# Performance work log

Measured on AMD Instinct MI355X. Metric: run time of the kernel, lower is better.

Reference implementation:

```python
import jax, jax.numpy as jnp
import numpy as np

DEGREE = 10

def _chebyshev_basis(x, degree):
    # x: [B, F] -> basis: [B, F, degree+1] via T0=1, T1=t, Tk=2t*T_{k-1}-T_{k-2}
    t = jnp.tanh(x)
    polys = [jnp.ones_like(t), t]
    for _ in range(2, degree + 1):
        polys.append(2.0 * t * polys[-1] - polys[-2])
    return jnp.stack(polys, axis=-1)

def setup_inputs() -> dict:
    key = jax.random.key(0)
    k1, k2, k3, k4 = jax.random.split(key, 4)
    B, F_IN, F_OUT, D = 8192, 1024, 1024, DEGREE
    x = jax.random.normal(k1, (B, F_IN), dtype=jnp.float32)
    coeff_mean = jax.random.normal(k2, (F_IN, F_OUT, D + 1), dtype=jnp.float32) * 0.05
    coeff_log_var = jnp.full((F_IN, F_OUT, D + 1), -5.0, dtype=jnp.float32)
    base_weight = jax.random.normal(k3, (F_IN, F_OUT), dtype=jnp.float32) * 0.05
    # reparameterization noise, n_samples=1
    eps = jax.random.normal(k4, (1, F_IN, F_OUT, D + 1), dtype=jnp.float32)
    return {"x": x, "coeff_mean": coeff_mean, "coeff_log_var": coeff_log_var,
            "base_weight": base_weight, "eps": eps}

def reference(x, coeff_mean, coeff_log_var, base_weight, eps):
    basis = _chebyshev_basis(x, DEGREE)                      # [B, F_in, D+1]
    std = jnp.exp(0.5 * coeff_log_var)                       # [F_in, F_out, D+1]
    coeffs = coeff_mean[None] + eps * std[None]              # [S, F_in, F_out, D+1]
    poly_out = jnp.einsum('bin,sion->bo', basis, coeffs) / coeffs.shape[0]
    linear_out = x @ base_weight
    # KL with prior_mean=0, prior_var=1 (prior_scale=1.0)
    var = jnp.exp(coeff_log_var)
    kl = 0.5 * jnp.sum(var + coeff_mean ** 2 - 1.0 - coeff_log_var)
    return poly_out + linear_out, kl
```

## Files before the change

### kernel.cpp

```cpp
#include <hip/hip_runtime.h>

#define MDIM 8192
#define NDIM 1024
#define FIN  1024
#define DP1  11
#define KDIM 11264
#define KHALF 5632
#define ROWB 22528
#define HOFS 2883584u
#define FGOFS 1441792u
#define NT 88
#define NITER 44

typedef __attribute__((ext_vector_type(8))) short short8;
typedef __attribute__((ext_vector_type(4))) float float4v;
typedef const __attribute__((address_space(1))) unsigned int* gptr_t;
typedef __attribute__((address_space(3))) unsigned int* lptr_t;

__device__ __forceinline__ unsigned int pk2(float a, float b) {
  unsigned int ua = __float_as_uint(a), ub = __float_as_uint(b);
  ua += 0x7FFFu + ((ua >> 16) & 1u);
  ub += 0x7FFFu + ((ub >> 16) & 1u);
  return __builtin_amdgcn_perm(ub, ua, 0x07060302);
}

__device__ __forceinline__ float fast_tanh(float x) {
  float e = __expf(2.f * x);
  return 1.f - 2.f / (e + 1.f);
}

struct Cheb { float t, T2, T3, T4, T5, T6, T7, T8, T9, T10; };
__device__ __forceinline__ Cheb cheb_eval(float x) {
  Cheb c;
  c.t = fast_tanh(x);
  const float t2 = 2.f * c.t;
  c.T2 = t2 * c.t - 1.f;
  c.T3 = t2 * c.T2 - c.t;
  c.T4 = t2 * c.T3 - c.T2;
  c.T5 = t2 * c.T4 - c.T3;
  c.T6 = t2 * c.T5 - c.T4;
  c.T7 = t2 * c.T6 - c.T5;
  c.T8 = t2 * c.T7 - c.T6;
  c.T9 = t2 * c.T8 - c.T7;
  c.T10 = t2 * c.T9 - c.T8;
  return c;
}

__device__ __forceinline__ void pack_pair(float xa, float xb, unsigned int* w) {
  Cheb a = cheb_eval(xa), b = cheb_eval(xb);
  w[0] = pk2(a.t, a.T2);  w[1] = pk2(a.T3, a.T4); w[2] = pk2(a.T5, a.T6);
  w[3] = pk2(a.T7, a.T8); w[4] = pk2(a.T9, a.T10); w[5] = pk2(xa, b.t);
  w[6] = pk2(b.T2, b.T3); w[7] = pk2(b.T4, b.T5);  w[8] = pk2(b.T6, b.T7);
  w[9] = pk2(b.T8, b.T9); w[10] = pk2(b.T10, xb);
}

__global__ __launch_bounds__(256) void prep_A_kernel(const float* __restrict__ x,
                                                     unsigned int* __restrict__ A) {
  __shared__ unsigned int rowbuf[5632];
  const int row = blockIdx.x;
  const int tid = threadIdx.x;
  float4 xv = ((const float4*)(x + (size_t)row * FIN))[tid];
  unsigned int w[22];
  pack_pair(xv.x, xv.y, w);
  pack_pair(xv.z, xv.w, w + 11);
#pragma unroll
  for (int j = 0; j < 22; j++) rowbuf[tid * 22 + j] = w[j];
  __syncthreads();
  uint2* dst = (uint2*)((char*)A + (size_t)row * ROWB);
  const uint2* src = (const uint2*)rowbuf;
#pragma unroll
  for (int j = 0; j < 11; j++) dst[tid + j * 256] = src[tid + j * 256];
}

__global__ __launch_bounds__(256) void prep_B_kernel(const float4* __restrict__ mean4,
    const float4* __restrict__ lv4, const float* __restrict__ W,
    const float4* __restrict__ eps4, unsigned short* __restrict__ Bt,
    float* __restrict__ kl_out, float* __restrict__ bias) {
  __shared__ float cf[2816];
  __shared__ unsigned int pkb[5632];
  __shared__ float wsum[4];
  const int tid = threadIdx.x;
  const int g = blockIdx.x >> 3;
  const int po = blockIdx.x & 7;
  float klp = 0.f;
  float biasAcc = 0.f;
#pragma unroll 1
  for (int pr = 0; pr < 4; ++pr) {
#pragma unroll
    for (int f = 0; f < 2; ++f) {
      const int i = g * 8 + pr * 2 + f;
      const size_t b4 = (size_t)i * 2816 + po * 352;
#pragma unroll
      for (int qq = 0; qq < 2; ++qq) {
        const int idx = qq * 256 + tid;
        if (idx < 352) {
          float4 m = mean4[b4 + idx];
          float4 l = lv4[b4 + idx];
          float4 e = eps4[b4 + idx];
          float s0 = __expf(0.5f * l.x), s1 = __expf(0.5f * l.y);
          float s2 = __expf(0.5f * l.z), s3 = __expf(0.5f * l.w);
          float4 c;
          c.x = fmaf(e.x, s0, m.x); c.y = fmaf(e.y, s1, m.y);
          c.z = fmaf(e.z, s2, m.z); c.w = fmaf(e.w, s3, m.w);
          klp += (s0 * s0 + m.x * m.x - 1.f - l.x) + (s1 * s1 + m.y * m.y - 1.f - l.y)
               + (s2 * s2 + m.z * m.z - 1.f - l.z) + (s3 * s3 + m.w * m.w - 1.f - l.w);
          ((float4*)cf)[f * 352 + idx] = c;
        }
      }
    }
    __syncthreads();
    if (tid < 128) {
      const int o = tid;
      const float* ca = &cf[o * DP1];
      const float* cb = &cf[1408 + o * DP1];
      const float wa = W[(size_t)(g * 8 + pr * 2) * NDIM + po * 128 + o];
      const float wb = W[(size_t)(g * 8 + pr * 2 + 1) * NDIM + po * 128 + o];
      biasAcc += ca[0] + cb[0];
      unsigned int* dq = &pkb[o * 44 + pr * 11];
      dq[0] = pk2(ca[1], ca[2]); dq[1] = pk2(ca[3], ca[4]); dq[2] = pk2(ca[5], ca[6]);
      dq[3] = pk2(ca[7], ca[8]); dq[4] = pk2(ca[9], ca[10]); dq[5] = pk2(wa, cb[1]);
      dq[6] = pk2(cb[2], cb[3]); dq[7] = pk2(cb[4], cb[5]); dq[8] = pk2(cb[6], cb[7]);
      dq[9] = pk2(cb[8], cb[9]); dq[10] = pk2(cb[10], wb);
    }
    __syncthreads();
  }
#pragma unroll
  for (int it = 0; it < 6; ++it) {
    const int cc = it * 256 + tid;
    if (cc < 1408) {
      const int o = cc / 11, c = cc - o * 11;
      uint4 v = *(const uint4*)&pkb[o * 44 + c * 4];
      *(uint4*)((char*)Bt + (size_t)(po * 128 + o) * ROWB + g * 176 + c * 16) = v;
    }
  }
  if (tid < 128) atomicAdd(&bias[po * 128 + tid], biasAcc);
#pragma unroll
  for (int off = 32; off > 0; off >>= 1) klp += __shfl_down(klp, off, 64);
  if ((tid & 63) == 0) wsum[tid >> 6] = klp;
  __syncthreads();
  if (tid == 0) atomicAdd(kl_out, 0.5f * (wsum[0] + wsum[1] + wsum[2] + wsum[3]));
}

#define VMW(N) asm volatile("s_waitcnt vmcnt(" #N ")" ::: "memory")

#define STG_A(p, fg, t) do {                                                              \
    __builtin_amdgcn_global_load_lds((gptr_t)(gA + baseAlo + (fg) * FGOFS + (unsigned)(t) * 128u), \
        (lptr_t)(ldsp + (p) * 65536 + (fg) * 8192 + dA), 16, 0, 0);                       \
    __builtin_amdgcn_global_load_lds((gptr_t)(gA + baseAhi + (fg) * FGOFS + (unsigned)(t) * 128u), \
        (lptr_t)(ldsp + (p) * 65536 + 16384 + (fg) * 8192 + dA), 16, 0, 0);               \
  } while (0)

#define STG_B(p, h, t) do {                                                               \
    __builtin_amdgcn_global_load_lds((gptr_t)(gB + baseB0 + (h) * HOFS + (unsigned)(t) * 128u), \
        (lptr_t)(ldsp + (p) * 65536 + 32768 + (h) * 16384 + dA), 16, 0, 0);               \
    __builtin_amdgcn_global_load_lds((gptr_t)(gB + baseB1 + (h) * HOFS + (unsigned)(t) * 128u), \
        (lptr_t)(ldsp + (p) * 65536 + 32768 + (h) * 16384 + 8192 + dA), 16, 0, 0);        \
  } while (0)

#define PH(p, f, STG_STMT, WAIT_STMT) do {                                                \
    const char* ap_ = ldsp + (p) * 65536 + aBase + (f) * 4096;                            \
    short8 a00 = *(const short8*)(ap_ + offk0);                                           \
    short8 a01 = *(const short8*)(ap_ + offk1);                                           \
    short8 a10 = *(const short8*)(ap_ + 2048 + offk0);                                    \
    short8 a11 = *(const short8*)(ap_ + 2048 + offk1);                                    \
    if ((f) == 0) {                                                                       \
      const char* bp_ = ldsp + (p) * 65536 + bBase;                                       \
      bfr[0][0] = *(const short8*)(bp_ + offk0);        bfr[0][1] = *(const short8*)(bp_ + offk1); \
      bfr[1][0] = *(const short8*)(bp_ + 2048 + offk0); bfr[1][1] = *(const short8*)(bp_ + 2048 + offk1); \
      bfr[2][0] = *(const short8*)(bp_ + 4096 + offk0); bfr[2][1] = *(const short8*)(bp_ + 4096 + offk1); \
      bfr[3][0] = *(const short8*)(bp_ + 6144 + offk0); bfr[3][1] = *(const short8*)(bp_ + 6144 + offk1); \
    }                                                                                     \
    STG_STMT;                                                                             \
    WAIT_STMT;                                                                            \
    __builtin_amdgcn_sched_barrier(0);                                                    \
    __builtin_amdgcn_s_barrier();                                                         \
    __builtin_amdgcn_sched_barrier(0);                                                    \
    __builtin_amdgcn_s_setprio(1);                                                        \
    _Pragma("unroll")                                                                     \
    for (int n_ = 0; n_ < 4; ++n_) {                                                      \
      acc[2 * (f)][n_]     = __builtin_amdgcn_mfma_f32_16x16x32_bf16(a00, bfr[n_][0], acc[2 * (f)][n_], 0, 0, 0);     \
      acc[2 * (f)][n_]     = __builtin_amdgcn_mfma_f32_16x16x32_bf16(a01, bfr[n_][1], acc[2 * (f)][n_], 0, 0, 0);     \
      acc[2 * (f) + 1][n_] = __builtin_amdgcn_mfma_f32_16x16x32_bf16(a10, bfr[n_][0], acc[2 * (f) + 1][n_], 0, 0, 0); \
      acc[2 * (f) + 1][n_] = __builtin_amdgcn_mfma_f32_16x16x32_bf16(a11, bfr[n_][1], acc[2 * (f) + 1][n_], 0, 0, 0); \
    }                                                                                     \
    __builtin_amdgcn_s_setprio(0);                                                        \
  } while (0)

__global__ __launch_bounds__(512, 2) void gemm_kernel(const unsigned short* __restrict__ A,
    const unsigned short* __restrict__ Bt, const float* __restrict__ bias,
    float* __restrict__ C) {
  __shared__ char lds[131072];
  char* ldsp = (char*)lds;
  const int tid = threadIdx.x;
  const int lane = tid & 63;
  const int wid = tid >> 6;
  const int wr = wid >> 2;
  const int wc = wid & 3;
  const int q = lane >> 4;
  const int r = lane & 15;
  const int bid = blockIdx.x;
  const int nt_ = bid & 3;
  const int kh = (bid >> 2) & 1;
  const int mt = bid >> 3;
  const int gm0 = mt * 256;
  const int gn0 = nt_ * 256;
  const unsigned kbyte0 = (unsigned)kh * KHALF * 2;

  const char* gA = (const char*)A;
  const char* gB = (const char*)Bt;

  const int srow = tid >> 3;
  const int scol = ((tid & 7) ^ (srow & 7)) << 4;
  const unsigned baseAlo = (unsigned)(gm0 + srow) * ROWB + kbyte0 + scol;
  const unsigned baseAhi = baseAlo + 128u * ROWB;
  const unsigned baseB0  = (unsigned)(gn0 + srow) * ROWB + kbyte0 + scol;
  const unsigned baseB1  = (unsigned)(gn0 + 64 + srow) * ROWB + kbyte0 + scol;
  const int dA = tid * 16;

  const int s7 = r & 7;
  const int offk0 = ((q ^ s7) << 4);
  const int offk1 = (((q + 4) ^ s7) << 4);
  const int aBase = wr * 16384 + r * 128;
  const int bBase = 32768 + (wc >> 1) * 16384 + ((wc & 1) * 64 + r) * 128;

  float4v acc[8][4];
#pragma unroll
  for (int m = 0; m < 8; m++)
#pragma unroll
    for (int n = 0; n < 4; n++) acc[m][n] = (float4v){0.f, 0.f, 0.f, 0.f};
  short8 bfr[4][2];

  STG_A(0, 0, 0); STG_A(0, 1, 0); STG_B(0, 0, 0); STG_B(0, 1, 0);
  STG_B(1, 0, 1); STG_B(1, 1, 1);
  VMW(4);
  __builtin_amdgcn_sched_barrier(0);
  __builtin_amdgcn_s_barrier();
  __builtin_amdgcn_sched_barrier(0);

#pragma unroll 1
  for (int i = 0; i < NITER - 1; ++i) {
    const int t1 = 2 * i + 1, t2 = 2 * i + 2, t3 = 2 * i + 3;
    PH(0, 0, STG_A(1, 0, t1), ;);
    PH(0, 1, STG_A(1, 1, t1), ;);
    PH(0, 2, STG_B(0, 0, t2), ;);
    PH(0, 3, STG_B(0, 1, t2), VMW(4));
    PH(1, 0, STG_A(0, 0, t2), ;);
    PH(1, 1, STG_A(0, 1, t2), ;);
    PH(1, 2, STG_B(1, 0, t3), ;);
    PH(1, 3, STG_B(1, 1, t3), VMW(4));
  }
  PH(0, 0, STG_A(1, 0, NT - 1), ;);
  PH(0, 1, STG_A(1, 1, NT - 1), ;);
  PH(0, 2, ;, ;);
  PH(0, 3, ;, VMW(0));
  PH(1, 0, ;, ;);
  PH(1, 1, ;, ;);
  PH(1, 2, ;, ;);
  PH(1, 3, ;, ;);

  float bv[4] = {0.f, 0.f, 0.f, 0.f};
  if (kh == 0) {
    const float* bp = bias + gn0 + wc * 64 + r;
#pragma unroll
    for (int n = 0; n < 4; n++) bv[n] = bp[n * 16];
  }
  float* Cb = C + (size_t)(gm0 + wr * 128) * NDIM + (gn0 + wc * 64);
#pragma unroll
  for (int m = 0; m < 8; m++)
#pragma unroll
    for (int n = 0; n < 4; n++)
#pragma unroll
      for (int v = 0; v < 4; v++)
        atomicAdd(&Cb[(size_t)(m * 16 + q * 4 + v) * NDIM + (n * 16 + r)], acc[m][n][v] + bv[n]);
}

extern "C" void kernel_launch(void* const* d_in, const int* in_sizes, int n_in,
                              void* d_out, int out_size, void* d_ws, size_t ws_size,
                              hipStream_t stream) {
  const float* x    = (const float*)d_in[0];
  const float* mean = (const float*)d_in[1];
  const float* lv   = (const float*)d_in[2];
  const float* W    = (const float*)d_in[3];
  const float* eps  = (const float*)d_in[4];
  float* out = (float*)d_out;

  unsigned short* Abf = (unsigned short*)d_ws;
  unsigned short* Bt  = (unsigned short*)((char*)d_ws + (size_t)MDIM * ROWB);
  float* bias = (float*)((char*)d_ws + (size_t)MDIM * ROWB + (size_t)NDIM * ROWB);
  float* kl = out + (size_t)MDIM * NDIM;

  hipMemsetAsync(out, 0, ((size_t)MDIM * NDIM + 1) * sizeof(float), stream);
  hipMemsetAsync(bias, 0, NDIM * sizeof(float), stream);
  prep_A_kernel<<<MDIM, 256, 0, stream>>>(x, (unsigned int*)Abf);
  prep_B_kernel<<<1024, 256, 0, stream>>>((const float4*)mean, (const float4*)lv, W,
                                          (const float4*)eps, Bt, kl, bias);
  gemm_kernel<<<256, 512, 0, stream>>>(Abf, Bt, bias, out);
}
```

Baseline: 413.0 us.

## Software-pipeline LDS fragment reads into double-buffered registers ahead of MFMA

Restructures the main loop so the A fragments for the next sub-phase are loaded from LDS into a second register set right after each barrier, before the MFMAs of the current sub-phase are issued. B fragments for the next LDS buffer are fetched after the last MFMA of each half-iteration. This aims to hide LDS read latency behind matrix-core work instead of stalling on it at the start of every phase. It adds 16 more live vector registers per thread under a 512-thread, 2-block launch bound, which risks spills or reduced occupancy, and it makes the read-after-barrier ordering more delicate.

```diff
diff --git a/kernel.cpp b/kernel.cpp
--- a/kernel.cpp
+++ b/kernel.cpp
@@ -157,33 +157,56 @@
         (lptr_t)(ldsp + (p) * 65536 + 32768 + (h) * 16384 + 8192 + dA), 16, 0, 0);        \
   } while (0)
 
-#define PH(p, f, STG_STMT, WAIT_STMT) do {                                                \
-    const char* ap_ = ldsp + (p) * 65536 + aBase + (f) * 4096;                            \
-    short8 a00 = *(const short8*)(ap_ + offk0);                                           \
-    short8 a01 = *(const short8*)(ap_ + offk1);                                           \
-    short8 a10 = *(const short8*)(ap_ + 2048 + offk0);                                    \
-    short8 a11 = *(const short8*)(ap_ + 2048 + offk1);                                    \
-    if ((f) == 0) {                                                                       \
-      const char* bp_ = ldsp + (p) * 65536 + bBase;                                       \
-      bfr[0][0] = *(const short8*)(bp_ + offk0);        bfr[0][1] = *(const short8*)(bp_ + offk1); \
-      bfr[1][0] = *(const short8*)(bp_ + 2048 + offk0); bfr[1][1] = *(const short8*)(bp_ + 2048 + offk1); \
-      bfr[2][0] = *(const short8*)(bp_ + 4096 + offk0); bfr[2][1] = *(const short8*)(bp_ + 4096 + offk1); \
-      bfr[3][0] = *(const short8*)(bp_ + 6144 + offk0); bfr[3][1] = *(const short8*)(bp_ + 6144 + offk1); \
+#define PRF_A(pn, fn, R) do {                                                             \
+    const char* apn_ = ldsp + (pn) * 65536 + aBase + (fn) * 4096;                         \
+    R[0] = *(const short8*)(apn_ + offk0);                                                \
+    R[1] = *(const short8*)(apn_ + offk1);                                                \
+    R[2] = *(const short8*)(apn_ + 2048 + offk0);                                         \
+    R[3] = *(const short8*)(apn_ + 2048 + offk1);                                         \
+  } while (0)
+
+#define PRF_B(pn) do {                                                                    \
+    const char* bpn_ = ldsp + (pn) * 65536 + bBase;                                       \
+    bfr[0][0] = *(const short8*)(bpn_ + offk0);        bfr[0][1] = *(const short8*)(bpn_ + offk1); \
+    bfr[1][0] = *(const short8*)(bpn_ + 2048 + offk0); bfr[1][1] = *(const short8*)(bpn_ + 2048 + offk1); \
+    bfr[2][0] = *(const short8*)(bpn_ + 4096 + offk0); bfr[2][1] = *(const short8*)(bpn_ + 4096 + offk1); \
+    bfr[3][0] = *(const short8*)(bpn_ + 6144 + offk0); bfr[3][1] = *(const short8*)(bpn_ + 6144 + offk1); \
+  } while (0)
+
+#define MMA(fc, R) do {                                                                   \
+    __builtin_amdgcn_s_setprio(1);                                                        \
+    _Pragma("unroll")                                                                     \
+    for (int n_ = 0; n_ < 4; ++n_) {                                                      \
+      acc[2 * (fc)][n_]     = __builtin_amdgcn_mfma_f32_16x16x32_bf16(R[0], bfr[n_][0], acc[2 * (fc)][n_], 0, 0, 0);     \
+      acc[2 * (fc)][n_]     = __builtin_amdgcn_mfma_f32_16x16x32_bf16(R[1], bfr[n_][1], acc[2 * (fc)][n_], 0, 0, 0);     \
+      acc[2 * (fc) + 1][n_] = __builtin_amdgcn_mfma_f32_16x16x32_bf16(R[2], bfr[n_][0], acc[2 * (fc) + 1][n_], 0, 0, 0); \
+      acc[2 * (fc) + 1][n_] = __builtin_amdgcn_mfma_f32_16x16x32_bf16(R[3], bfr[n_][1], acc[2 * (fc) + 1][n_], 0, 0, 0); \
     }                                                                                     \
-    STG_STMT;                                                                             \
-    WAIT_STMT;                                                                            \
+    __builtin_amdgcn_s_setprio(0);                                                        \
+  } while (0)
+
+#define SBAR do {                                                                         \
     __builtin_amdgcn_sched_barrier(0);                                                    \
     __builtin_amdgcn_s_barrier();                                                         \
     __builtin_amdgcn_sched_barrier(0);                                                    \
-    __builtin_amdgcn_s_setprio(1);                                                        \
-    _Pragma("unroll")                                                                     \
-    for (int n_ = 0; n_ < 4; ++n_) {                                                      \
-      acc[2 * (f)][n_]     = __builtin_amdgcn_mfma_f32_16x16x32_bf16(a00, bfr[n_][0], acc[2 * (f)][n_], 0, 0, 0);     \
-      acc[2 * (f)][n_]     = __builtin_amdgcn_mfma_f32_16x16x32_bf16(a01, bfr[n_][1], acc[2 * (f)][n_], 0, 0, 0);     \
-      acc[2 * (f) + 1][n_] = __builtin_amdgcn_mfma_f32_16x16x32_bf16(a10, bfr[n_][0], acc[2 * (f) + 1][n_], 0, 0, 0); \
-      acc[2 * (f) + 1][n_] = __builtin_amdgcn_mfma_f32_16x16x32_bf16(a11, bfr[n_][1], acc[2 * (f) + 1][n_], 0, 0, 0); \
-    }                                                                                     \
-    __builtin_amdgcn_s_setprio(0);                                                        \
+  } while (0)
+
+#define BODY(fc, RC, pn, fn, RN, STG_STMT, WAIT_STMT) do {                                \
+    STG_STMT;                                                                             \
+    WAIT_STMT;                                                                            \
+    SBAR;                                                                                 \
+    PRF_A(pn, fn, RN);                                                                    \
+    MMA(fc, RC);                                                                          \
+  } while (0)
+
+#define BODYB(fc, RC, pn, fn, RN, STG_STMT, WAIT_STMT) do {                               \
+    STG_STMT;                                                                             \
+    WAIT_STMT;                                                                            \
+    SBAR;                                                                                 \
+    PRF_A(pn, fn, RN);                                                                    \
+    MMA(fc, RC);                                                                          \
+    __builtin_amdgcn_sched_barrier(0);                                                    \
+    PRF_B(pn);                                                                            \
   } while (0)
 
 __global__ __launch_bounds__(512, 2) void gemm_kernel(const unsigned short* __restrict__ A,
@@ -229,34 +252,36 @@
 #pragma unroll
     for (int n = 0; n < 4; n++) acc[m][n] = (float4v){0.f, 0.f, 0.f, 0.f};
   short8 bfr[4][2];
+  short8 aRA[4], aRB[4];
 
   STG_A(0, 0, 0); STG_A(0, 1, 0); STG_B(0, 0, 0); STG_B(0, 1, 0);
   STG_B(1, 0, 1); STG_B(1, 1, 1);
   VMW(4);
-  __builtin_amdgcn_sched_barrier(0);
-  __builtin_amdgcn_s_barrier();
-  __builtin_amdgcn_sched_barrier(0);
+  SBAR;
+  PRF_A(0, 0, aRA);
+  PRF_B(0);
 
 #pragma unroll 1
   for (int i = 0; i < NITER - 1; ++i) {
     const int t1 = 2 * i + 1, t2 = 2 * i + 2, t3 = 2 * i + 3;
-    PH(0, 0, STG_A(1, 0, t1), ;);
-    PH(0, 1, STG_A(1, 1, t1), ;);
-    PH(0, 2, STG_B(0, 0, t2), ;);
-    PH(0, 3, STG_B(0, 1, t2), VMW(4));
-    PH(1, 0, STG_A(0, 0, t2), ;);
-    PH(1, 1, STG_A(0, 1, t2), ;);
-    PH(1, 2, STG_B(1, 0, t3), ;);
-    PH(1, 3, STG_B(1, 1, t3), VMW(4));
+    BODY (0, aRA, 0, 1, aRB, STG_A(1, 0, t1), ;);
+    BODY (1, aRB, 0, 2, aRA, STG_A(1, 1, t1), ;);
+    BODY (2, aRA, 0, 3, aRB, STG_B(0, 0, t2), ;);
+    BODYB(3, aRB, 1, 0, aRA, STG_B(0, 1, t2), VMW(4));
+    BODY (0, aRA, 1, 1, aRB, STG_A(0, 0, t2), ;);
+    BODY (1, aRB, 1, 2, aRA, STG_A(0, 1, t2), ;);
+    BODY (2, aRA, 1, 3, aRB, STG_B(1, 0, t3), ;);
+    BODYB(3, aRB, 0, 0, aRA, STG_B(1, 1, t3), VMW(4));
   }
-  PH(0, 0, STG_A(1, 0, NT - 1), ;);
-  PH(0, 1, STG_A(1, 1, NT - 1), ;);
-  PH(0, 2, ;, ;);
-  PH(0, 3, ;, VMW(0));
-  PH(1, 0, ;, ;);
-  PH(1, 1, ;, ;);
-  PH(1, 2, ;, ;);
-  PH(1, 3, ;, ;);
+  BODY (0, aRA, 0, 1, aRB, STG_A(1, 0, NT - 1), ;);
+  BODY (1, aRB, 0, 2, aRA, STG_A(1, 1, NT - 1), ;);
+  BODY (2, aRA, 0, 3, aRB, ;, ;);
+  BODYB(3, aRB, 1, 0, aRA, ;, VMW(0));
+  BODY (0, aRA, 1, 1, aRB, ;, ;);
+  BODY (1, aRB, 1, 2, aRA, ;, ;);
+  BODY (2, aRA, 1, 3, aRB, ;, ;);
+  SBAR;
+  MMA(3, aRB);
 
   float bv[4] = {0.f, 0.f, 0.f, 0.f};
   if (kh == 0) {
```

New measurement: 419.6 us. Within noise of the previous version (+1.6%).
